# Kernel optimization log

Measured on AMD Instinct MI355X. Metric: run time of the kernel, lower is better.

Reference implementation:

```python
import jax, jax.numpy as jnp
import numpy as np

N, E, F_IN, C1, H1, C2, NUM_CLASSES, NUM_GRAPHS = 50000, 800000, 128, 64, 4, 128, 5, 32
NEG_SLOPE = 0.2


def gat_conv(x, W, att_src, att_dst, bias, src, dst, heads, out_ch):
    # x: [N, in], W: [in, heads*out_ch], att_*: [heads, out_ch], bias: [heads*out_ch]
    n = x.shape[0]
    h = (x @ W).reshape(n, heads, out_ch)                      # [N,H,C]
    a_src = jnp.sum(h * att_src, axis=-1)                      # [N,H]
    a_dst = jnp.sum(h * att_dst, axis=-1)                      # [N,H]
    alpha = a_src[src] + a_dst[dst]                            # [E,H]
    alpha = jax.nn.leaky_relu(alpha, NEG_SLOPE)
    # scatter-softmax over incoming edges of each dst node (every node has a self-loop)
    amax = jax.ops.segment_max(alpha, dst, num_segments=n)
    ealpha = jnp.exp(alpha - amax[dst])
    denom = jax.ops.segment_sum(ealpha, dst, num_segments=n)
    alpha = ealpha / (denom[dst] + 1e-16)                      # [E,H]
    msg = h[src] * alpha[..., None]                            # [E,H,C]
    out = jax.ops.segment_sum(msg, dst, num_segments=n)        # [N,H,C]
    return out.reshape(n, heads * out_ch) + bias


def setup_inputs() -> dict:
    key = jax.random.key(0)
    ks = jax.random.split(key, 12)
    x = jax.random.normal(ks[0], (N, F_IN), dtype=jnp.float32)
    edge_index = jax.random.randint(ks[1], (2, E), 0, N, dtype=jnp.int64)
    batch = jnp.sort(jax.random.randint(ks[2], (N,), 0, NUM_GRAPHS, dtype=jnp.int64))
    s1 = 1.0 / np.sqrt(F_IN)
    s2 = 1.0 / np.sqrt(H1 * C1)
    s3 = 1.0 / np.sqrt(C2)
    return {
        "x": x,
        "edge_index": edge_index,
        "batch": batch,
        "W1": jax.random.normal(ks[3], (F_IN, H1 * C1), dtype=jnp.float32) * s1,
        "att_src1": jax.random.normal(ks[4], (H1, C1), dtype=jnp.float32) * s1,
        "att_dst1": jax.random.normal(ks[5], (H1, C1), dtype=jnp.float32) * s1,
        "b1": jnp.zeros((H1 * C1,), dtype=jnp.float32),
        "W2": jax.random.normal(ks[6], (H1 * C1, C2), dtype=jnp.float32) * s2,
        "att_src2": jax.random.normal(ks[7], (1, C2), dtype=jnp.float32) * s2,
        "att_dst2": jax.random.normal(ks[8], (1, C2), dtype=jnp.float32) * s2,
        "b2": jnp.zeros((C2,), dtype=jnp.float32),
        "lin_w": jax.random.normal(ks[9], (C2, NUM_CLASSES), dtype=jnp.float32) * s3,
        "lin_b": jnp.zeros((NUM_CLASSES,), dtype=jnp.float32),
    }


def reference(x, edge_index, batch, W1, att_src1, att_dst1, b1, W2, att_src2, att_dst2, b2, lin_w, lin_b):
    n = x.shape[0]
    # PyG GATConv adds self-loops by default
    loops = jnp.arange(n, dtype=edge_index.dtype)
    src = jnp.concatenate([edge_index[0], loops])
    dst = jnp.concatenate([edge_index[1], loops])
    h = jax.nn.elu(gat_conv(x, W1, att_src1, att_dst1, b1, src, dst, H1, C1))
    h = jax.nn.elu(gat_conv(h, W2, att_src2, att_dst2, b2, src, dst, 1, C2))
    # global_mean_pool over graphs
    sums = jax.ops.segment_sum(h, batch, num_segments=NUM_GRAPHS)          # [G,C2]
    counts = jax.ops.segment_sum(jnp.ones((n,), h.dtype), batch, num_segments=NUM_GRAPHS)
    pooled = sums / jnp.maximum(counts, 1.0)[:, None]
    # dropout is identity in eval mode
    return pooled @ lin_w + lin_b
```

## Files before the change

### kernel.cpp

```cpp
#include <hip/hip_runtime.h>
#include <math.h>

#define NEG_SLOPE 0.2f

__device__ inline float lrelu(float x) { return x > 0.f ? x : NEG_SLOPE * x; }

typedef __attribute__((ext_vector_type(8))) _Float16 f16x8;
typedef __attribute__((ext_vector_type(4))) float f32x4;
typedef __attribute__((ext_vector_type(2))) float f32x2;
typedef __attribute__((ext_vector_type(4))) _Float16 h16x4;
typedef __attribute__((ext_vector_type(2))) _Float16 h16x2;

__global__ void convW_k(const float* __restrict__ W1, const float* __restrict__ W2,
                        _Float16* __restrict__ BT1, _Float16* __restrict__ BT2)
{
    int i = blockIdx.x * blockDim.x + threadIdx.x;
    if (i < 32768) {
        int n = i >> 7, k = i & 127;
        BT1[(size_t)n * 128 + k] = (_Float16)W1[(size_t)k * 256 + n];
    } else {
        int idx = i - 32768;
        int n = idx >> 8, k = idx & 255;
        BT2[(size_t)n * 256 + k] = (_Float16)W2[(size_t)k * 128 + n];
    }
}

template<int N, int K, int H, bool AF16>
__launch_bounds__(256)
__global__ void gemm_fused(const void* __restrict__ A, const _Float16* __restrict__ BT,
                           unsigned char* __restrict__ HB, const float* __restrict__ att_s,
                           const float* __restrict__ att_d, float* __restrict__ aS,
                           float* __restrict__ aD, int M)
{
    constexpr int ITERS = K / 32;
    constexpr int WN = N / 4;
    constexpr int NT = WN / 16;
    constexpr int NCH = (N * 4) / 256;
    __shared__ unsigned short As[64 * 40] __attribute__((aligned(16)));
    __shared__ unsigned short Bs[N * 40] __attribute__((aligned(16)));
    const int t = threadIdx.x;
    const int wave = t >> 6, lane = t & 63;
    const int quad = lane >> 4, l15 = lane & 15;
    const int rowBase = blockIdx.x * 64;

    f32x4 acc[4][NT];
#pragma unroll
    for (int mi = 0; mi < 4; ++mi)
#pragma unroll
        for (int ni = 0; ni < NT; ++ni)
            acc[mi][ni] = (f32x4){0.f, 0.f, 0.f, 0.f};

    const int ar = t >> 2;
    const int ak = (t & 3) << 3;
    const int bc = (t * NCH) >> 2;
    const int bks = (t * NCH) & 3;

    for (int it = 0; it < ITERS; ++it) {
        {
            int gr = rowBase + ar;
            f16x8 hv;
#pragma unroll
            for (int j = 0; j < 8; ++j) hv[j] = (_Float16)0.f;
            if (gr < M) {
                if constexpr (AF16) {
                    hv = *(const f16x8*)((const _Float16*)A + (size_t)gr * K + it * 32 + ak);
                } else {
                    const float* ap = (const float*)A + (size_t)gr * K + it * 32 + ak;
                    float4 v0 = *(const float4*)ap;
                    float4 v1 = *(const float4*)(ap + 4);
                    hv[0] = (_Float16)v0.x; hv[1] = (_Float16)v0.y;
                    hv[2] = (_Float16)v0.z; hv[3] = (_Float16)v0.w;
                    hv[4] = (_Float16)v1.x; hv[5] = (_Float16)v1.y;
                    hv[6] = (_Float16)v1.z; hv[7] = (_Float16)v1.w;
                }
            }
            *(f16x8*)&As[ar * 40 + ak] = hv;
        }
        {
            const _Float16* bp = BT + (size_t)bc * K + it * 32 + bks * 8;
            unsigned short* dp = &Bs[bc * 40 + bks * 8];
#pragma unroll
            for (int j = 0; j < NCH; ++j)
                *(f16x8*)(dp + j * 8) = *(const f16x8*)(bp + j * 8);
        }
        __syncthreads();
        f16x8 af[4], bfr[NT];
#pragma unroll
        for (int mi = 0; mi < 4; ++mi)
            af[mi] = *(const f16x8*)&As[(mi * 16 + l15) * 40 + quad * 8];
#pragma unroll
        for (int ni = 0; ni < NT; ++ni)
            bfr[ni] = *(const f16x8*)&Bs[(wave * WN + ni * 16 + l15) * 40 + quad * 8];
#pragma unroll
        for (int mi = 0; mi < 4; ++mi)
#pragma unroll
            for (int ni = 0; ni < NT; ++ni)
                acc[mi][ni] = __builtin_amdgcn_mfma_f32_16x16x32_f16(
                    af[mi], bfr[ni], acc[mi][ni], 0, 0, 0);
        __syncthreads();
    }
    float asv[NT], adv[NT];
#pragma unroll
    for (int ni = 0; ni < NT; ++ni) {
        int col = wave * WN + ni * 16 + l15;
        asv[ni] = att_s[col];
        adv[ni] = att_d[col];
    }
#pragma unroll
    for (int mi = 0; mi < 4; ++mi) {
#pragma unroll
        for (int r = 0; r < 4; ++r) {
            int row = rowBase + mi * 16 + quad * 4 + r;
            bool ok = row < M;
            float ss = 0.f, sd = 0.f;
#pragma unroll
            for (int ni = 0; ni < NT; ++ni) {
                float v = acc[mi][ni][r];
                ss += v * asv[ni];
                sd += v * adv[ni];
            }
#pragma unroll
            for (int ni = 0; ni < NT; ni += 2) {
                int pk = __builtin_amdgcn_cvt_pk_fp8_f32(acc[mi][ni][r],
                                                         acc[mi][ni + 1][r], 0, false);
                if (ok) {
                    HB[(size_t)row * N + wave * WN + ni * 16 + l15] =
                        (unsigned char)(pk & 0xff);
                    HB[(size_t)row * N + wave * WN + (ni + 1) * 16 + l15] =
                        (unsigned char)((pk >> 8) & 0xff);
                }
            }
#pragma unroll
            for (int off = 8; off > 0; off >>= 1) {
                ss += __shfl_xor(ss, off);
                sd += __shfl_xor(sd, off);
            }
            if (ok && l15 == 0) {
                if (H == 4) {
                    aS[row * 4 + wave] = ss;
                    aD[row * 4 + wave] = sd;
                } else {
                    atomicAdd(&aS[row], ss);
                    atomicAdd(&aD[row], sd);
                }
            }
        }
    }
}

__global__ void count_k(const int* __restrict__ dst, int* __restrict__ counts, int E, int Nn)
{
    int e = blockIdx.x * blockDim.x + threadIdx.x;
    if (e >= E + Nn) return;
    int d = (e < E) ? dst[e] : (e - E);
    atomicAdd(&counts[d], 1);
}

__global__ void scan1_k(const int* __restrict__ counts, int* __restrict__ partial,
                        int* __restrict__ bsum, int Nn)
{
    __shared__ int sh[256];
    int i = blockIdx.x * 256 + threadIdx.x;
    int v = (i < Nn) ? counts[i] : 0;
    sh[threadIdx.x] = v;
    __syncthreads();
#pragma unroll
    for (int o = 1; o < 256; o <<= 1) {
        int t = (threadIdx.x >= o) ? sh[threadIdx.x - o] : 0;
        __syncthreads();
        sh[threadIdx.x] += t;
        __syncthreads();
    }
    if (i < Nn) partial[i] = sh[threadIdx.x] - v;
    if (threadIdx.x == 255) bsum[blockIdx.x] = sh[255];
}

__global__ void scan2_k(int* __restrict__ bsum, int nb)
{
    __shared__ int sh[256];
    int v = (threadIdx.x < nb) ? bsum[threadIdx.x] : 0;
    sh[threadIdx.x] = v;
    __syncthreads();
#pragma unroll
    for (int o = 1; o < 256; o <<= 1) {
        int t = (threadIdx.x >= o) ? sh[threadIdx.x - o] : 0;
        __syncthreads();
        sh[threadIdx.x] += t;
        __syncthreads();
    }
    if (threadIdx.x < nb) bsum[threadIdx.x] = sh[threadIdx.x] - v;
}

__global__ void scan3_k(const int* __restrict__ partial, const int* __restrict__ bsum,
                        int* __restrict__ rowptr, int* __restrict__ cursor, int Nn, int ET)
{
    int i = blockIdx.x * 256 + threadIdx.x;
    if (i < Nn) {
        int v = partial[i] + bsum[i >> 8];
        rowptr[i] = v;
        cursor[i] = v;
    }
    if (i == Nn) rowptr[Nn] = ET;
}

__global__ void build_k(const int* __restrict__ src, const int* __restrict__ dst,
                        int* __restrict__ cursor, int* __restrict__ esrc, int E, int Nn)
{
    int e = blockIdx.x * blockDim.x + threadIdx.x;
    if (e >= E + Nn) return;
    int s, d;
    if (e < E) { s = src[e]; d = dst[e]; } else { s = e - E; d = s; }
    int pos = atomicAdd(&cursor[d], 1);
    esrc[pos] = s;
}

__global__ void gather1_k(const int* __restrict__ rp, const int* __restrict__ esrc,
                          const unsigned char* __restrict__ hb, const float* __restrict__ aS,
                          const float* __restrict__ aD, const float* __restrict__ bias,
                          _Float16* __restrict__ out, int Nn)
{
    int d = blockIdx.x * 4 + (threadIdx.x >> 6);
    int lane = threadIdx.x & 63;
    if (d >= Nn) return;
    int c4 = lane << 2;
    int head = lane >> 4;
    int p0 = __builtin_amdgcn_readfirstlane(rp[d]);
    int p1 = __builtin_amdgcn_readfirstlane(rp[d + 1]);
    float adh = aD[d * 4 + head];
    const float* aSh = aS + head;
    float m = -1e30f, den = 0.f;
    float ax = 0.f, ay = 0.f, az = 0.f, aw = 0.f;
    int p = p0;
    for (; p + 8 <= p1; p += 8) {
        int s[8];
        float l[8];
#pragma unroll
        for (int j = 0; j < 8; ++j) s[j] = __builtin_amdgcn_readfirstlane(esrc[p + j]);
#pragma unroll
        for (int j = 0; j < 8; ++j) l[j] = lrelu(aSh[s[j] * 4] + adh);
        float lm = l[0];
#pragma unroll
        for (int j = 1; j < 8; ++j) lm = fmaxf(lm, l[j]);
        if (lm > m) {
            float r = __expf(m - lm);
            ax *= r; ay *= r; az *= r; aw *= r; den *= r;
            m = lm;
        }
        unsigned int v[8];
#pragma unroll
        for (int j = 0; j < 8; ++j)
            v[j] = *(const unsigned int*)&hb[(size_t)s[j] * 256 + c4];
#pragma unroll
        for (int j = 0; j < 8; ++j) {
            float w = __expf(l[j] - m);
            den += w;
            f32x2 lo = __builtin_amdgcn_cvt_pk_f32_fp8((int)v[j], false);
            f32x2 hi = __builtin_amdgcn_cvt_pk_f32_fp8((int)v[j], true);
            ax += lo[0] * w;
            ay += lo[1] * w;
            az += hi[0] * w;
            aw += hi[1] * w;
        }
    }
    for (; p < p1; ++p) {
        int s0 = __builtin_amdgcn_readfirstlane(esrc[p]);
        float l0 = lrelu(aSh[s0 * 4] + adh);
        if (l0 > m) {
            float r = __expf(m - l0);
            ax *= r; ay *= r; az *= r; aw *= r; den *= r;
            m = l0;
        }
        float w0 = __expf(l0 - m);
        den += w0;
        unsigned int v0 = *(const unsigned int*)&hb[(size_t)s0 * 256 + c4];
        f32x2 lo = __builtin_amdgcn_cvt_pk_f32_fp8((int)v0, false);
        f32x2 hi = __builtin_amdgcn_cvt_pk_f32_fp8((int)v0, true);
        ax += lo[0] * w0; ay += lo[1] * w0;
        az += hi[0] * w0; aw += hi[1] * w0;
    }
    float inv = 1.f / (den + 1e-16f);
    float4 b4 = *(const float4*)&bias[c4];
    float rx, ry, rz, rw;
    rx = ax * inv + b4.x; rx = rx > 0.f ? rx : expm1f(rx);
    ry = ay * inv + b4.y; ry = ry > 0.f ? ry : expm1f(ry);
    rz = az * inv + b4.z; rz = rz > 0.f ? rz : expm1f(rz);
    rw = aw * inv + b4.w; rw = rw > 0.f ? rw : expm1f(rw);
    h16x4 r16;
    r16[0] = (_Float16)rx; r16[1] = (_Float16)ry;
    r16[2] = (_Float16)rz; r16[3] = (_Float16)rw;
    *(h16x4*)&out[(size_t)d * 256 + c4] = r16;
}

__global__ void gather2_k(const int* __restrict__ rp, const int* __restrict__ esrc,
                          const unsigned char* __restrict__ hb, const float* __restrict__ aS,
                          const float* __restrict__ aD, _Float16* __restrict__ out, int Nn)
{
    int d = blockIdx.x * 4 + (threadIdx.x >> 6);
    int lane = threadIdx.x & 63;
    if (d >= Nn) return;
    int c2 = lane << 1;
    int p0 = __builtin_amdgcn_readfirstlane(rp[d]);
    int p1 = __builtin_amdgcn_readfirstlane(rp[d + 1]);
    float adh = aD[d];
    float m = -1e30f, den = 0.f;
    float ax = 0.f, ay = 0.f;
    int p = p0;
    for (; p + 8 <= p1; p += 8) {
        int s[8];
        float l[8];
#pragma unroll
        for (int j = 0; j < 8; ++j) s[j] = __builtin_amdgcn_readfirstlane(esrc[p + j]);
#pragma unroll
        for (int j = 0; j < 8; ++j) l[j] = lrelu(aS[s[j]] + adh);
        float lm = l[0];
#pragma unroll
        for (int j = 1; j < 8; ++j) lm = fmaxf(lm, l[j]);
        if (lm > m) {
            float r = __expf(m - lm);
            ax *= r; ay *= r; den *= r;
            m = lm;
        }
        unsigned short v[8];
#pragma unroll
        for (int j = 0; j < 8; ++j)
            v[j] = *(const unsigned short*)&hb[(size_t)s[j] * 128 + c2];
#pragma unroll
        for (int j = 0; j < 8; ++j) {
            float w = __expf(l[j] - m);
            den += w;
            f32x2 lo = __builtin_amdgcn_cvt_pk_f32_fp8((int)v[j], false);
            ax += lo[0] * w;
            ay += lo[1] * w;
        }
    }
    for (; p < p1; ++p) {
        int s0 = __builtin_amdgcn_readfirstlane(esrc[p]);
        float l0 = lrelu(aS[s0] + adh);
        if (l0 > m) {
            float r = __expf(m - l0);
            ax *= r; ay *= r; den *= r;
            m = l0;
        }
        float w0 = __expf(l0 - m);
        den += w0;
        unsigned short v0 = *(const unsigned short*)&hb[(size_t)s0 * 128 + c2];
        f32x2 lo = __builtin_amdgcn_cvt_pk_f32_fp8((int)v0, false);
        ax += lo[0] * w0;
        ay += lo[1] * w0;
    }
    float inv = 1.f / (den + 1e-16f);
    h16x2 r16;
    r16[0] = (_Float16)(ax * inv);
    r16[1] = (_Float16)(ay * inv);
    *(h16x2*)&out[(size_t)d * 128 + c2] = r16;
}

__global__ void pool_k(const _Float16* __restrict__ o2, const float* __restrict__ b2,
                       const int* __restrict__ batch, float* __restrict__ sums, int Nn, int C)
{
    int c = threadIdx.x;
    int n0 = blockIdx.x * 64;
    int n1 = min(n0 + 64, Nn);
    float local = 0.f;
    int gcur = batch[n0];
    float bc = b2[c];
    for (int n = n0; n < n1; ++n) {
        int g = batch[n];
        if (g != gcur) {
            atomicAdd(&sums[gcur * C + c], local);
            local = 0.f;
            gcur = g;
        }
        float v = (float)o2[(size_t)n * C + c] + bc;
        local += v > 0.f ? v : expm1f(v);
    }
    atomicAdd(&sums[gcur * C + c], local);
}

__global__ void final_k(const float* __restrict__ sums, const int* __restrict__ batch,
                        const float* __restrict__ lin_w, const float* __restrict__ lin_b,
                        float* __restrict__ out, int Nn, int G, int C, int NC)
{
    __shared__ float inv[64];
    int t = threadIdx.x;
    if (t < G) {
        int lo = 0, hi = Nn;
        while (lo < hi) { int mid = (lo + hi) >> 1; if (batch[mid] < t) lo = mid + 1; else hi = mid; }
        int lb = lo;
        lo = 0; hi = Nn;
        while (lo < hi) { int mid = (lo + hi) >> 1; if (batch[mid] < t + 1) lo = mid + 1; else hi = mid; }
        int cnt = lo - lb;
        inv[t] = 1.f / fmaxf((float)cnt, 1.f);
    }
    __syncthreads();
    if (t < G * NC) {
        int g = t / NC, k = t % NC;
        float acc = 0.f;
        for (int c = 0; c < C; ++c) acc += sums[g * C + c] * lin_w[c * NC + k];
        out[t] = acc * inv[g] + lin_b[k];
    }
}

extern "C" void kernel_launch(void* const* d_in, const int* in_sizes, int n_in,
                              void* d_out, int out_size, void* d_ws, size_t ws_size,
                              hipStream_t stream)
{
    const float* x      = (const float*)d_in[0];
    const int*   eidx   = (const int*)d_in[1];
    const int*   batch  = (const int*)d_in[2];
    const float* W1     = (const float*)d_in[3];
    const float* att_s1 = (const float*)d_in[4];
    const float* att_d1 = (const float*)d_in[5];
    const float* b1     = (const float*)d_in[6];
    const float* W2     = (const float*)d_in[7];
    const float* att_s2 = (const float*)d_in[8];
    const float* att_d2 = (const float*)d_in[9];
    const float* b2     = (const float*)d_in[10];
    const float* lin_w  = (const float*)d_in[11];
    const float* lin_b  = (const float*)d_in[12];

    const int Nn  = in_sizes[2];
    const int E   = in_sizes[1] / 2;
    const int H1_ = 4, C1_ = 64, C2_ = 128, G = 32, NC = 5;
    const int D1 = H1_ * C1_;
    const int ET = E + Nn;

    const int* srcp = eidx;
    const int* dstp = eidx + E;

    float* ws = (float*)d_ws;
    size_t off = 0;
    auto alloc = [&](size_t n) { float* p = ws + off; off += n; return p; };
    _Float16* o1h = (_Float16*)alloc((size_t)Nn * D1 / 2);
    _Float16* o2h = (_Float16*)alloc((size_t)Nn * C2_ / 2);
    float* aS1  = alloc((size_t)Nn * H1_);
    float* aD1  = alloc((size_t)Nn * H1_);
    float* aS2  = alloc(Nn);
    float* aD2  = alloc(Nn);
    float* sums = alloc((size_t)G * C2_);
    _Float16* BT1 = (_Float16*)alloc(D1 * 128 / 2);
    _Float16* BT2 = (_Float16*)alloc(C2_ * 256 / 2);
    unsigned char* hb1 = (unsigned char*)alloc((size_t)Nn * D1 / 4);
    unsigned char* hb2 = (unsigned char*)alloc((size_t)Nn * C2_ / 4);
    int* iws    = (int*)(ws + off);
    int* counts = iws;
    int* partial= iws + Nn;
    int* rowptr = iws + 2 * Nn;
    int* cursor = iws + 3 * Nn + 1;
    int* bsum   = iws + 4 * Nn + 1;
    int* esrc   = iws + 4 * Nn + 1 + 256;

    const int NB = (Nn + 255) / 256;
    const int GB = (Nn + 63) / 64;

    hipMemsetAsync(counts, 0, (size_t)Nn * 4, stream);
    hipMemsetAsync(aS2, 0, (size_t)2 * Nn * 4, stream);
    count_k<<<(ET + 255) / 256, 256, 0, stream>>>(dstp, counts, E, Nn);
    scan1_k<<<NB, 256, 0, stream>>>(counts, partial, bsum, Nn);
    scan2_k<<<1, 256, 0, stream>>>(bsum, NB);
    scan3_k<<<(Nn + 256) / 256, 256, 0, stream>>>(partial, bsum, rowptr, cursor, Nn, ET);
    build_k<<<(ET + 255) / 256, 256, 0, stream>>>(srcp, dstp, cursor, esrc, E, Nn);

    convW_k<<<256, 256, 0, stream>>>(W1, W2, BT1, BT2);

    gemm_fused<256, 128, 4, false><<<GB, 256, 0, stream>>>(x, BT1, hb1, att_s1, att_d1,
                                                           aS1, aD1, Nn);
    gather1_k<<<(Nn + 3) / 4, 256, 0, stream>>>(rowptr, esrc, hb1, aS1, aD1, b1, o1h, Nn);

    gemm_fused<128, 256, 1, true><<<GB, 256, 0, stream>>>(o1h, BT2, hb2, att_s2, att_d2,
                                                          aS2, aD2, Nn);
    gather2_k<<<(Nn + 3) / 4, 256, 0, stream>>>(rowptr, esrc, hb2, aS2, aD2, o2h, Nn);

    hipMemsetAsync(sums, 0, (size_t)G * C2_ * 4, stream);
    pool_k<<<GB, C2_, 0, stream>>>(o2h, b2, batch, sums, Nn, C2_);
    final_k<<<1, 256, 0, stream>>>(sums, batch, lin_w, lin_b, (float*)d_out, Nn, G, C2_, NC);
}
```

Before: 365.7 us.

## Build CSR in two bucketed passes and store edge sources as 16-bit

Replaces the single-pass CSR build, which did random atomics on per-node cursors, with two passes. First a coarse binning pass sends each edge to a bucket of 64 destination nodes, packing the source and the local destination offset into one int. Then a per-bucket pass places edges at their final positions with local atomics. The edge-source array also shrinks to uint16, which cuts index bandwidth in both gather kernels. The cost is an extra kernel launch and a temporary buffer, and the packing only works while the node count stays below 65536.

```diff
diff --git a/kernel.cpp b/kernel.cpp
--- a/kernel.cpp
+++ b/kernel.cpp
@@ -192,29 +192,46 @@
 }
 
 __global__ void scan3_k(const int* __restrict__ partial, const int* __restrict__ bsum,
-                        int* __restrict__ rowptr, int* __restrict__ cursor, int Nn, int ET)
+                        int* __restrict__ rowptr, int* __restrict__ cursor,
+                        int* __restrict__ ccursor, int Nn, int ET)
 {
     int i = blockIdx.x * 256 + threadIdx.x;
     if (i < Nn) {
         int v = partial[i] + bsum[i >> 8];
         rowptr[i] = v;
         cursor[i] = v;
+        if ((i & 63) == 0) ccursor[i >> 6] = v;
     }
     if (i == Nn) rowptr[Nn] = ET;
 }
 
-__global__ void build_k(const int* __restrict__ src, const int* __restrict__ dst,
-                        int* __restrict__ cursor, int* __restrict__ esrc, int E, int Nn)
+__global__ void binpass_k(const int* __restrict__ src, const int* __restrict__ dst,
+                          int* __restrict__ ccursor, int* __restrict__ tmp, int E, int Nn)
 {
     int e = blockIdx.x * blockDim.x + threadIdx.x;
     if (e >= E + Nn) return;
     int s, d;
     if (e < E) { s = src[e]; d = dst[e]; } else { s = e - E; d = s; }
-    int pos = atomicAdd(&cursor[d], 1);
-    esrc[pos] = s;
-}
-
-__global__ void gather1_k(const int* __restrict__ rp, const int* __restrict__ esrc,
+    int pos = atomicAdd(&ccursor[d >> 6], 1);
+    tmp[pos] = s | ((d & 63) << 16);
+}
+
+__global__ void fine_k(const int* __restrict__ rowptr, const int* __restrict__ tmp,
+                       int* __restrict__ cursor, unsigned short* __restrict__ esrc, int Nn)
+{
+    int b = blockIdx.x;
+    int n0 = b << 6;
+    int base = rowptr[n0];
+    int end = rowptr[min(n0 + 64, Nn)];
+    for (int i = base + (int)threadIdx.x; i < end; i += 256) {
+        int v = tmp[i];
+        int node = n0 + (v >> 16);
+        int pos = atomicAdd(&cursor[node], 1);
+        esrc[pos] = (unsigned short)(v & 0xffff);
+    }
+}
+
+__global__ void gather1_k(const int* __restrict__ rp, const unsigned short* __restrict__ esrc,
                           const unsigned char* __restrict__ hb, const float* __restrict__ aS,
                           const float* __restrict__ aD, const float* __restrict__ bias,
                           _Float16* __restrict__ out, int Nn)
@@ -291,7 +308,7 @@
     *(h16x4*)&out[(size_t)d * 256 + c4] = r16;
 }
 
-__global__ void gather2_k(const int* __restrict__ rp, const int* __restrict__ esrc,
+__global__ void gather2_k(const int* __restrict__ rp, const unsigned short* __restrict__ esrc,
                           const unsigned char* __restrict__ hb, const float* __restrict__ aS,
                           const float* __restrict__ aD, _Float16* __restrict__ out, int Nn)
 {
@@ -424,6 +441,7 @@
     const int H1_ = 4, C1_ = 64, C2_ = 128, G = 32, NC = 5;
     const int D1 = H1_ * C1_;
     const int ET = E + Nn;
+    const int NBUCK = (Nn + 63) >> 6;
 
     const int* srcp = eidx;
     const int* dstp = eidx + E;
@@ -448,7 +466,9 @@
     int* rowptr = iws + 2 * Nn;
     int* cursor = iws + 3 * Nn + 1;
     int* bsum   = iws + 4 * Nn + 1;
-    int* esrc   = iws + 4 * Nn + 1 + 256;
+    int* ccursor= iws + 4 * Nn + 1 + 256;
+    int* tmp    = iws + 4 * Nn + 1 + 256 + 1024;
+    unsigned short* esrc = (unsigned short*)(tmp + ET);
 
     const int NB = (Nn + 255) / 256;
     const int GB = (Nn + 63) / 64;
@@ -458,8 +478,10 @@
     count_k<<<(ET + 255) / 256, 256, 0, stream>>>(dstp, counts, E, Nn);
     scan1_k<<<NB, 256, 0, stream>>>(counts, partial, bsum, Nn);
     scan2_k<<<1, 256, 0, stream>>>(bsum, NB);
-    scan3_k<<<(Nn + 256) / 256, 256, 0, stream>>>(partial, bsum, rowptr, cursor, Nn, ET);
-    build_k<<<(ET + 255) / 256, 256, 0, stream>>>(srcp, dstp, cursor, esrc, E, Nn);
+    scan3_k<<<(Nn + 256) / 256, 256, 0, stream>>>(partial, bsum, rowptr, cursor,
+                                                  ccursor, Nn, ET);
+    binpass_k<<<(ET + 255) / 256, 256, 0, stream>>>(srcp, dstp, ccursor, tmp, E, Nn);
+    fine_k<<<NBUCK, 256, 0, stream>>>(rowptr, tmp, cursor, esrc, Nn);
 
     convW_k<<<256, 256, 0, stream>>>(W1, W2, BT1, BT2);
 
```

Result: slower. 559.0 us (+52.9%).
